# Optimization experiments

Measured on AMD Instinct MI355X. Metric: run time of the kernel, lower is better.

The kernel has to match this reference:

```python
import jax, jax.numpy as jnp
import numpy as np

HEADS = 4
DIM_HEAD = 32
CHUNK = 1024
GROUPS = 8
EPS = 1e-5


def setup_inputs() -> dict:
    key = jax.random.key(0)
    k1, k2, k3 = jax.random.split(key, 3)
    b, dim, h, w = 8, 64, 96, 96
    inner = HEADS * DIM_HEAD  # 128
    x = jax.random.normal(k1, (b, dim, h, w), dtype=jnp.float32)
    W_qkv = jax.random.normal(k2, (3 * inner, dim), dtype=jnp.float32) * (1.0 / np.sqrt(dim))
    W_out = jax.random.normal(k3, (dim, inner), dtype=jnp.float32) * (1.0 / np.sqrt(inner))
    b_out = jnp.zeros((dim,), dtype=jnp.float32)
    gamma = jnp.ones((dim,), dtype=jnp.float32)
    beta = jnp.zeros((dim,), dtype=jnp.float32)
    return {"x": x, "W_qkv": W_qkv, "W_out": W_out, "b_out": b_out,
            "gamma": gamma, "beta": beta}


def reference(x, W_qkv, W_out, b_out, gamma, beta):
    b, c, h, w = x.shape
    n = h * w
    nch = n // CHUNK  # number of full chunks (n chosen divisible by CHUNK)
    d = DIM_HEAD
    BH = b * HEADS

    # 1x1 conv (no bias) == matmul over channel dim
    xf = x.reshape(b, c, n)
    qkv = jnp.einsum('oc,bcn->bon', W_qkv, xf)          # [b, 3*inner, n]
    q, k, v = jnp.split(qkv, 3, axis=1)                  # each [b, inner, n]

    def chunkify(t):
        # [b, inner, n] -> [BH, nch, d, CHUNK]; slicing i:i+CHUNK on last axis
        # equals reshaping n -> (nch, CHUNK) in order.
        return t.reshape(BH, d, nch, CHUNK).transpose(0, 2, 1, 3)

    qc, kc, vc = chunkify(q), chunkify(k), chunkify(v)

    qs = jax.nn.softmax(qc, axis=-1)  # softmax over chunk spatial positions
    ks = jax.nn.softmax(kc, axis=-2)  # softmax over head channels

    # context = k_chunk^T @ v_chunk : [BH, nch, CHUNK, CHUNK]
    ctx = jnp.einsum('gkdi,gkdj->gkij', ks, vc)
    # chunk_out = q_chunk @ context : [BH, nch, d, CHUNK]
    out = jnp.einsum('gkdi,gkij->gkdj', qs, ctx)

    # concat chunks back along spatial dim, reshape to image layout
    out = out.transpose(0, 2, 1, 3).reshape(b, HEADS * d, h, w)

    # to_out: 1x1 conv with bias, then GroupNorm(8, dim)
    y = jnp.einsum('oc,bchw->bohw', W_out, out) + b_out[None, :, None, None]

    yg = y.reshape(b, GROUPS, c // GROUPS, h, w)
    mu = jnp.mean(yg, axis=(2, 3, 4), keepdims=True)
    var = jnp.var(yg, axis=(2, 3, 4), keepdims=True)
    yn = ((yg - mu) * jax.lax.rsqrt(var + EPS)).reshape(b, c, h, w)
    return yn * gamma[None, :, None, None] + beta[None, :, None, None]
```

## Files before the change

### kernel.cpp

```cpp
#include <hip/hip_runtime.h>
#include <hip/hip_bf16.h>

#define N_POS 9216
#define NCHUNK 9
#define BATCH 8
#define CDIM 64
#define HEADS 4
#define EPS 1e-5f

#define PPART_SZ ((size_t)32 * NCHUNK * 1024)
#define NPART 8
#define UBF_BYTES ((size_t)BATCH * NCHUNK * 64 * 128 * 2)
#define WBF_BYTES ((size_t)384 * 64 * 2)

typedef __attribute__((ext_vector_type(8))) short short8;
typedef __attribute__((ext_vector_type(4))) float f32x4;

static __device__ inline unsigned pk2(float a, float b) {
    __hip_bfloat162 h2(__float2bfloat16(a), __float2bfloat16(b));
    return *reinterpret_cast<unsigned*>(&h2);
}
static __device__ inline float bf2f(short s) {
    union { unsigned u; float f; } c; c.u = ((unsigned)(unsigned short)s) << 16; return c.f;
}

__global__ __launch_bounds__(256) void wprep_kernel(const float* __restrict__ Wqkv,
        __hip_bfloat16* __restrict__ wbf, float* __restrict__ stats) {
    int i = blockIdx.x * 256 + threadIdx.x;
    if (i < 6144) {
        float4 v = ((const float4*)Wqkv)[i];
        uint2 u; u.x = pk2(v.x, v.y); u.y = pk2(v.z, v.w);
        ((uint2*)wbf)[i] = u;
    }
    if (i < 128) stats[i] = 0.f;
}

__global__ __launch_bounds__(256) void qkp_kernel(const float* __restrict__ x,
        const __hip_bfloat16* __restrict__ wbf, float* __restrict__ Pparts) {
    int bx = blockIdx.x;
    int b  = blockIdx.y;
    int ck = bx >> 3, pt = bx & 7;
    __shared__ __align__(16) char lraw[36864];
    __hip_bfloat16 (*xs)[72]  = (__hip_bfloat16(*)[72])lraw;
    __hip_bfloat16 (*skT)[72] = (__hip_bfloat16(*)[72])lraw;
    int t = threadIdx.x, w = t >> 6, l = t & 63;
    int l15 = l & 15, quad = l >> 4;

    f32x4 pac[2][2];
    pac[0][0] = (f32x4){0,0,0,0}; pac[0][1] = (f32x4){0,0,0,0};
    pac[1][0] = (f32x4){0,0,0,0}; pac[1][1] = (f32x4){0,0,0,0};

    for (int half = 0; half < 2; ++half) {
        int n0 = bx * 128 + half * 64;
        {
            int p = t & 63, cbase = (t >> 6) * 16;
            const float* xb = x + (size_t)b * CDIM * N_POS + n0 + p;
            #pragma unroll
            for (int j = 0; j < 16; j += 4) {
                float v0 = xb[(size_t)(cbase + j + 0) * N_POS];
                float v1 = xb[(size_t)(cbase + j + 1) * N_POS];
                float v2 = xb[(size_t)(cbase + j + 2) * N_POS];
                float v3 = xb[(size_t)(cbase + j + 3) * N_POS];
                uint2 u; u.x = pk2(v0, v1); u.y = pk2(v2, v3);
                *reinterpret_cast<uint2*>(&xs[p][cbase + j]) = u;
            }
        }
        __syncthreads();

        f32x4 acc[4][4];
        #pragma unroll
        for (int mt = 0; mt < 4; ++mt)
            #pragma unroll
            for (int nt = 0; nt < 4; ++nt) acc[mt][nt] = (f32x4){0.f, 0.f, 0.f, 0.f};
        #pragma unroll
        for (int ks = 0; ks < 2; ++ks) {
            int k0 = ks * 32 + quad * 8;
            short8 av[4];
            #pragma unroll
            for (int mt = 0; mt < 4; ++mt)
                av[mt] = *reinterpret_cast<const short8*>(&xs[mt * 16 + l15][k0]);
            #pragma unroll
            for (int nt = 0; nt < 4; ++nt) {
                short8 bw = *reinterpret_cast<const short8*>(wbf + (size_t)(w * 64 + nt * 16 + l15) * 64 + k0);
                #pragma unroll
                for (int mt = 0; mt < 4; ++mt)
                    acc[mt][nt] = __builtin_amdgcn_mfma_f32_16x16x32_bf16(av[mt], bw, acc[mt][nt], 0, 0, 0);
            }
        }
        __syncthreads();

        #pragma unroll
        for (int nt = 0; nt < 4; ++nt) {
            int ch = w * 64 + nt * 16 + l15;
            #pragma unroll
            for (int mt = 0; mt < 4; ++mt) {
                uint2 u;
                u.x = pk2(acc[mt][nt][0], acc[mt][nt][1]);
                u.y = pk2(acc[mt][nt][2], acc[mt][nt][3]);
                *reinterpret_cast<uint2*>(&skT[ch][mt * 16 + quad * 4]) = u;
            }
        }
        __syncthreads();

        {
            int p = t & 63, h = t >> 6;
            float kr[32]; float mx = -1e30f;
            #pragma unroll
            for (int d = 0; d < 32; ++d) { kr[d] = bf2f(*(const short*)&skT[128 + h * 32 + d][p]); mx = fmaxf(mx, kr[d]); }
            float s = 0.f;
            #pragma unroll
            for (int d = 0; d < 32; ++d) { kr[d] = __expf(kr[d] - mx); s += kr[d]; }
            float is = 1.f / s;
            #pragma unroll
            for (int d = 0; d < 32; ++d) skT[128 + h * 32 + d][p] = __float2bfloat16(kr[d] * is);
            #pragma unroll
            for (int d = 0; d < 32; ++d) {
                float qv = bf2f(*(const short*)&skT[h * 32 + d][p]);
                skT[h * 32 + d][p] = __float2bfloat16(__expf(qv));
            }
        }
        __syncthreads();

        #pragma unroll
        for (int step = 0; step < 2; ++step) {
            int k0 = step * 32 + quad * 8;
            short8 bk[2];
            #pragma unroll
            for (int nt = 0; nt < 2; ++nt)
                bk[nt] = *reinterpret_cast<const short8*>(&skT[128 + w * 32 + nt * 16 + l15][k0]);
            #pragma unroll
            for (int mt = 0; mt < 2; ++mt) {
                short8 aq = *reinterpret_cast<const short8*>(&skT[w * 32 + mt * 16 + l15][k0]);
                pac[mt][0] = __builtin_amdgcn_mfma_f32_16x16x32_bf16(aq, bk[0], pac[mt][0], 0, 0, 0);
                pac[mt][1] = __builtin_amdgcn_mfma_f32_16x16x32_bf16(aq, bk[1], pac[mt][1], 0, 0, 0);
            }
        }
        __syncthreads();
    }

    float* Pp = Pparts + (size_t)pt * PPART_SZ + ((size_t)(b * 4 + w) * NCHUNK + ck) * 1024;
    #pragma unroll
    for (int mt = 0; mt < 2; ++mt)
        #pragma unroll
        for (int nt = 0; nt < 2; ++nt)
            #pragma unroll
            for (int r = 0; r < 4; ++r)
                Pp[(mt * 16 + quad * 4 + r) * 32 + nt * 16 + l15] = pac[mt][nt][r];
}

__global__ __launch_bounds__(256) void umat_kernel(const float* __restrict__ Wout,
        const float* __restrict__ Pparts, __hip_bfloat16* __restrict__ Ubf) {
    int ck = blockIdx.x, b = blockIdx.y, h = blockIdx.z;
    int bh = b * 4 + h;
    int t = threadIdx.x;
    __shared__ float Pl[32][32];
    __shared__ float iZ[32];
    size_t base4 = ((size_t)bh * NCHUNK + ck) * 256;
    {
        const float4* P0 = (const float4*)Pparts + base4 + t;
        float4 s = (float4){0.f, 0.f, 0.f, 0.f};
        #pragma unroll
        for (int j = 0; j < NPART; ++j) {
            float4 a = P0[j * (PPART_SZ / 4)];
            s.x += a.x; s.y += a.y; s.z += a.z; s.w += a.w;
        }
        ((float4*)Pl)[t] = s;
    }
    __syncthreads();
    if (t < 32) {
        float s = 0.f;
        #pragma unroll
        for (int c = 0; c < 32; ++c) s += Pl[t][c];
        iZ[t] = 1.f / s;
    }
    __syncthreads();
    int o = t & 63, wv = t >> 6;
    float wz[32];
    {
        const float4* wr = (const float4*)(Wout + (size_t)o * 128 + h * 32);
        #pragma unroll
        for (int j = 0; j < 8; ++j) {
            float4 f = wr[j];
            wz[j*4+0] = f.x * iZ[j*4+0]; wz[j*4+1] = f.y * iZ[j*4+1];
            wz[j*4+2] = f.z * iZ[j*4+2]; wz[j*4+3] = f.w * iZ[j*4+3];
        }
    }
    float ua[8];
    #pragma unroll
    for (int j = 0; j < 8; ++j) ua[j] = 0.f;
    for (int d = 0; d < 32; ++d) {
        float wd = wz[d];
        #pragma unroll
        for (int j = 0; j < 8; ++j) ua[j] += wd * Pl[d][wv * 8 + j];
    }
    uint4 up;
    up.x = pk2(ua[0], ua[1]); up.y = pk2(ua[2], ua[3]);
    up.z = pk2(ua[4], ua[5]); up.w = pk2(ua[6], ua[7]);
    __hip_bfloat16* Up = Ubf + ((size_t)(b * NCHUNK + ck) * 64 + o) * 128 + h * 32 + wv * 8;
    *reinterpret_cast<uint4*>(Up) = up;
}

__global__ __launch_bounds__(256) void vy_kernel(const float* __restrict__ x,
        const __hip_bfloat16* __restrict__ wbf, const __hip_bfloat16* __restrict__ Ubf,
        const float* __restrict__ bout, __hip_bfloat16* __restrict__ ybf,
        float* __restrict__ stats) {
    int bx = blockIdx.x;
    int b  = blockIdx.y;
    int ck = bx >> 3;
    int n0 = bx * 128;
    __shared__ __align__(16) char lraw[34816];
    __hip_bfloat16 (*xs)[72]    = (__hip_bfloat16(*)[72])lraw;
    __hip_bfloat16 (*vbuf)[136] = (__hip_bfloat16(*)[136])lraw;
    __shared__ float gsum[8], gsq[8];
    int t = threadIdx.x, w = t >> 6, l = t & 63;
    int l15 = l & 15, quad = l >> 4;
    if (t < 8) { gsum[t] = 0.f; gsq[t] = 0.f; }

    {
        int p = t & 127, cbase = (t >> 7) * 32;
        const float* xb = x + (size_t)b * CDIM * N_POS + n0 + p;
        #pragma unroll
        for (int j = 0; j < 32; j += 4) {
            float v0 = xb[(size_t)(cbase + j + 0) * N_POS];
            float v1 = xb[(size_t)(cbase + j + 1) * N_POS];
            float v2 = xb[(size_t)(cbase + j + 2) * N_POS];
            float v3 = xb[(size_t)(cbase + j + 3) * N_POS];
            uint2 u; u.x = pk2(v0, v1); u.y = pk2(v2, v3);
            *reinterpret_cast<uint2*>(&xs[p][cbase + j]) = u;
        }
    }
    __syncthreads();

    int nw = w * 32;
    {
        f32x4 vacc[8][2];
        #pragma unroll
        for (int mt = 0; mt < 8; ++mt) { vacc[mt][0] = (f32x4){0,0,0,0}; vacc[mt][1] = (f32x4){0,0,0,0}; }
        #pragma unroll
        for (int ks = 0; ks < 2; ++ks) {
            int k0 = ks * 32 + quad * 8;
            short8 bfr[2];
            #pragma unroll
            for (int nt = 0; nt < 2; ++nt)
                bfr[nt] = *reinterpret_cast<const short8*>(&xs[nw + nt * 16 + l15][k0]);
            #pragma unroll
            for (int mt = 0; mt < 8; ++mt) {
                short8 afr = *reinterpret_cast<const short8*>(wbf + (size_t)(256 + mt * 16 + l15) * 64 + k0);
                vacc[mt][0] = __builtin_amdgcn_mfma_f32_16x16x32_bf16(afr, bfr[0], vacc[mt][0], 0, 0, 0);
                vacc[mt][1] = __builtin_amdgcn_mfma_f32_16x16x32_bf16(afr, bfr[1], vacc[mt][1], 0, 0, 0);
            }
        }
        __syncthreads();

        #pragma unroll
        for (int mt = 0; mt < 8; ++mt)
            #pragma unroll
            for (int nt = 0; nt < 2; ++nt) {
                int p = nw + nt * 16 + l15;
                uint2 u;
                u.x = pk2(vacc[mt][nt][0], vacc[mt][nt][1]);
                u.y = pk2(vacc[mt][nt][2], vacc[mt][nt][3]);
                *reinterpret_cast<uint2*>(&vbuf[p][mt * 16 + quad * 4]) = u;
            }
    }
    __syncthreads();

    const __hip_bfloat16* Ub = Ubf + (size_t)(b * NCHUNK + ck) * 64 * 128;
    f32x4 acc[4][2];
    #pragma unroll
    for (int mt = 0; mt < 4; ++mt) { acc[mt][0] = (f32x4){0,0,0,0}; acc[mt][1] = (f32x4){0,0,0,0}; }
    #pragma unroll
    for (int ks = 0; ks < 4; ++ks) {
        int k0 = ks * 32 + quad * 8;
        short8 bf[2];
        #pragma unroll
        for (int nt = 0; nt < 2; ++nt)
            bf[nt] = *reinterpret_cast<const short8*>(&vbuf[nw + nt * 16 + l15][k0]);
        #pragma unroll
        for (int mt = 0; mt < 4; ++mt) {
            short8 af = *reinterpret_cast<const short8*>(Ub + (size_t)(mt * 16 + l15) * 128 + k0);
            acc[mt][0] = __builtin_amdgcn_mfma_f32_16x16x32_bf16(af, bf[0], acc[mt][0], 0, 0, 0);
            acc[mt][1] = __builtin_amdgcn_mfma_f32_16x16x32_bf16(af, bf[1], acc[mt][1], 0, 0, 0);
        }
    }
    float gsl[4], gql[4];
    #pragma unroll
    for (int mt = 0; mt < 4; ++mt) { gsl[mt] = 0.f; gql[mt] = 0.f; }
    __hip_bfloat16* yb = ybf + (size_t)b * CDIM * N_POS;
    int nbase = n0 + nw;
    #pragma unroll
    for (int mt = 0; mt < 4; ++mt) {
        float4 bo = *reinterpret_cast<const float4*>(bout + mt * 16 + quad * 4);
        const float* bop = reinterpret_cast<const float*>(&bo);
        #pragma unroll
        for (int nt = 0; nt < 2; ++nt) {
            int n = nbase + nt * 16 + l15;
            #pragma unroll
            for (int r = 0; r < 4; ++r) {
                int o = mt * 16 + quad * 4 + r;
                float val = acc[mt][nt][r] + bop[r];
                yb[(size_t)o * N_POS + n] = __float2bfloat16(val);
                gsl[mt] += val; gql[mt] += val * val;
            }
        }
    }
    #pragma unroll
    for (int off = 16; off >= 1; off >>= 1) {
        #pragma unroll
        for (int mt = 0; mt < 4; ++mt) {
            gsl[mt] += __shfl_xor(gsl[mt], off, 64);
            gql[mt] += __shfl_xor(gql[mt], off, 64);
        }
    }
    if (l == 0 || l == 32) {
        int qh = quad >> 1;
        #pragma unroll
        for (int mt = 0; mt < 4; ++mt) {
            atomicAdd(&gsum[2 * mt + qh], gsl[mt]);
            atomicAdd(&gsq[2 * mt + qh], gql[mt]);
        }
    }
    __syncthreads();
    if (t < 8) {
        atomicAdd(&stats[(b * 8 + t) * 2],     gsum[t]);
        atomicAdd(&stats[(b * 8 + t) * 2 + 1], gsq[t]);
    }
}

__global__ __launch_bounds__(256) void gn_kernel(const __hip_bfloat16* __restrict__ ybf,
        float* __restrict__ out, const float* __restrict__ stats,
        const float* __restrict__ gamma, const float* __restrict__ beta) {
    int bc = blockIdx.y;
    int c = bc & 63, b = bc >> 6;
    int g = c >> 3;
    float s = stats[(b * 8 + g) * 2], q = stats[(b * 8 + g) * 2 + 1];
    const float invN = 1.f / (8.f * N_POS);
    float mean = s * invN;
    float var = q * invN - mean * mean;
    float sc = rsqrtf(var + EPS);
    float ga = gamma[c] * sc;
    float be = beta[c] - mean * sc * gamma[c];
    size_t base = ((size_t)b * CDIM + c) * N_POS + (size_t)(blockIdx.x * 256 + threadIdx.x) * 4;
    uint2 u = *reinterpret_cast<const uint2*>(ybf + base);
    float4 v;
    v.x = bf2f((short)(u.x & 0xffff)); v.y = bf2f((short)(u.x >> 16));
    v.z = bf2f((short)(u.y & 0xffff)); v.w = bf2f((short)(u.y >> 16));
    v.x = v.x * ga + be; v.y = v.y * ga + be; v.z = v.z * ga + be; v.w = v.w * ga + be;
    *reinterpret_cast<float4*>(out + base) = v;
}

extern "C" void kernel_launch(void* const* d_in, const int* in_sizes, int n_in,
                              void* d_out, int out_size, void* d_ws, size_t ws_size,
                              hipStream_t stream) {
    const float* x     = (const float*)d_in[0];
    const float* Wqkv  = (const float*)d_in[1];
    const float* Wout  = (const float*)d_in[2];
    const float* bout  = (const float*)d_in[3];
    const float* gamma = (const float*)d_in[4];
    const float* beta  = (const float*)d_in[5];
    float* out = (float*)d_out;

    float* stats  = (float*)d_ws;
    float* Pparts = stats + 128;
    __hip_bfloat16* Ubf = (__hip_bfloat16*)(Pparts + NPART * PPART_SZ);
    __hip_bfloat16* wbf = (__hip_bfloat16*)((char*)Ubf + UBF_BYTES);
    __hip_bfloat16* ybf = (__hip_bfloat16*)((char*)wbf + WBF_BYTES);

    wprep_kernel<<<dim3(24), 256, 0, stream>>>(Wqkv, wbf, stats);
    qkp_kernel<<<dim3(72, BATCH), 256, 0, stream>>>(x, wbf, Pparts);
    umat_kernel<<<dim3(NCHUNK, BATCH, HEADS), 256, 0, stream>>>(Wout, Pparts, Ubf);
    vy_kernel<<<dim3(72, BATCH), 256, 0, stream>>>(x, wbf, Ubf, bout, ybf, stats);
    gn_kernel<<<dim3(9, 512), 256, 0, stream>>>(ybf, out, stats, gamma, beta);
}
```

Baseline: 125.6 us.

## Reduce chunk partials with atomics and fuse U-matrix build into vy kernel

qkp_kernel now atomically adds its partial 32x32 P tiles into a single zeroed buffer instead of writing eight separate partial slices. The separate umat_kernel is removed, and each vy_kernel block rebuilds the Wout-scaled U matrix for its chunk in shared memory. This drops one launch and the partial-sum and U round trips through global memory. The cost is atomic contention (eight blocks per target), a larger zeroing pass in wprep, redundant U computation in all eight blocks per chunk, and extra LDS in vy_kernel that may reduce occupancy.

```diff
diff --git a/kernel.cpp b/kernel.cpp
--- a/kernel.cpp
+++ b/kernel.cpp
@@ -8,9 +8,7 @@
 #define HEADS 4
 #define EPS 1e-5f
 
-#define PPART_SZ ((size_t)32 * NCHUNK * 1024)
-#define NPART 8
-#define UBF_BYTES ((size_t)BATCH * NCHUNK * 64 * 128 * 2)
+#define PSUM_SZ ((size_t)32 * NCHUNK * 1024)
 #define WBF_BYTES ((size_t)384 * 64 * 2)
 
 typedef __attribute__((ext_vector_type(8))) short short8;
@@ -25,21 +23,22 @@
 }
 
 __global__ __launch_bounds__(256) void wprep_kernel(const float* __restrict__ Wqkv,
-        __hip_bfloat16* __restrict__ wbf, float* __restrict__ stats) {
+        __hip_bfloat16* __restrict__ wbf, float* __restrict__ zbase) {
     int i = blockIdx.x * 256 + threadIdx.x;
     if (i < 6144) {
         float4 v = ((const float4*)Wqkv)[i];
         uint2 u; u.x = pk2(v.x, v.y); u.y = pk2(v.z, v.w);
         ((uint2*)wbf)[i] = u;
     }
-    if (i < 128) stats[i] = 0.f;
+    if (i < (128 + (int)PSUM_SZ) / 4)
+        ((float4*)zbase)[i] = (float4){0.f, 0.f, 0.f, 0.f};
 }
 
 __global__ __launch_bounds__(256) void qkp_kernel(const float* __restrict__ x,
-        const __hip_bfloat16* __restrict__ wbf, float* __restrict__ Pparts) {
+        const __hip_bfloat16* __restrict__ wbf, float* __restrict__ Psum) {
     int bx = blockIdx.x;
     int b  = blockIdx.y;
-    int ck = bx >> 3, pt = bx & 7;
+    int ck = bx >> 3;
     __shared__ __align__(16) char lraw[36864];
     __hip_bfloat16 (*xs)[72]  = (__hip_bfloat16(*)[72])lraw;
     __hip_bfloat16 (*skT)[72] = (__hip_bfloat16(*)[72])lraw;
@@ -138,72 +137,20 @@
         __syncthreads();
     }
 
-    float* Pp = Pparts + (size_t)pt * PPART_SZ + ((size_t)(b * 4 + w) * NCHUNK + ck) * 1024;
+    float* Pp = Psum + ((size_t)(b * 4 + w) * NCHUNK + ck) * 1024;
     #pragma unroll
     for (int mt = 0; mt < 2; ++mt)
         #pragma unroll
         for (int nt = 0; nt < 2; ++nt)
             #pragma unroll
             for (int r = 0; r < 4; ++r)
-                Pp[(mt * 16 + quad * 4 + r) * 32 + nt * 16 + l15] = pac[mt][nt][r];
-}
-
-__global__ __launch_bounds__(256) void umat_kernel(const float* __restrict__ Wout,
-        const float* __restrict__ Pparts, __hip_bfloat16* __restrict__ Ubf) {
-    int ck = blockIdx.x, b = blockIdx.y, h = blockIdx.z;
-    int bh = b * 4 + h;
-    int t = threadIdx.x;
-    __shared__ float Pl[32][32];
-    __shared__ float iZ[32];
-    size_t base4 = ((size_t)bh * NCHUNK + ck) * 256;
-    {
-        const float4* P0 = (const float4*)Pparts + base4 + t;
-        float4 s = (float4){0.f, 0.f, 0.f, 0.f};
-        #pragma unroll
-        for (int j = 0; j < NPART; ++j) {
-            float4 a = P0[j * (PPART_SZ / 4)];
-            s.x += a.x; s.y += a.y; s.z += a.z; s.w += a.w;
-        }
-        ((float4*)Pl)[t] = s;
-    }
-    __syncthreads();
-    if (t < 32) {
-        float s = 0.f;
-        #pragma unroll
-        for (int c = 0; c < 32; ++c) s += Pl[t][c];
-        iZ[t] = 1.f / s;
-    }
-    __syncthreads();
-    int o = t & 63, wv = t >> 6;
-    float wz[32];
-    {
-        const float4* wr = (const float4*)(Wout + (size_t)o * 128 + h * 32);
-        #pragma unroll
-        for (int j = 0; j < 8; ++j) {
-            float4 f = wr[j];
-            wz[j*4+0] = f.x * iZ[j*4+0]; wz[j*4+1] = f.y * iZ[j*4+1];
-            wz[j*4+2] = f.z * iZ[j*4+2]; wz[j*4+3] = f.w * iZ[j*4+3];
-        }
-    }
-    float ua[8];
-    #pragma unroll
-    for (int j = 0; j < 8; ++j) ua[j] = 0.f;
-    for (int d = 0; d < 32; ++d) {
-        float wd = wz[d];
-        #pragma unroll
-        for (int j = 0; j < 8; ++j) ua[j] += wd * Pl[d][wv * 8 + j];
-    }
-    uint4 up;
-    up.x = pk2(ua[0], ua[1]); up.y = pk2(ua[2], ua[3]);
-    up.z = pk2(ua[4], ua[5]); up.w = pk2(ua[6], ua[7]);
-    __hip_bfloat16* Up = Ubf + ((size_t)(b * NCHUNK + ck) * 64 + o) * 128 + h * 32 + wv * 8;
-    *reinterpret_cast<uint4*>(Up) = up;
+                atomicAdd(&Pp[(mt * 16 + quad * 4 + r) * 32 + nt * 16 + l15], pac[mt][nt][r]);
 }
 
 __global__ __launch_bounds__(256) void vy_kernel(const float* __restrict__ x,
-        const __hip_bfloat16* __restrict__ wbf, const __hip_bfloat16* __restrict__ Ubf,
-        const float* __restrict__ bout, __hip_bfloat16* __restrict__ ybf,
-        float* __restrict__ stats) {
+        const __hip_bfloat16* __restrict__ wbf, const float* __restrict__ Psum,
+        const float* __restrict__ Wout, const float* __restrict__ bout,
+        __hip_bfloat16* __restrict__ ybf, float* __restrict__ stats) {
     int bx = blockIdx.x;
     int b  = blockIdx.y;
     int ck = bx >> 3;
@@ -211,10 +158,56 @@
     __shared__ __align__(16) char lraw[34816];
     __hip_bfloat16 (*xs)[72]    = (__hip_bfloat16(*)[72])lraw;
     __hip_bfloat16 (*vbuf)[136] = (__hip_bfloat16(*)[136])lraw;
+    float (*Pl4)[32][32] = (float(*)[32][32])lraw;
+    __shared__ __align__(16) __hip_bfloat16 Ubuf[64][136];
+    __shared__ float iZ4[4][32];
     __shared__ float gsum[8], gsq[8];
     int t = threadIdx.x, w = t >> 6, l = t & 63;
     int l15 = l & 15, quad = l >> 4;
     if (t < 8) { gsum[t] = 0.f; gsq[t] = 0.f; }
+
+    {
+        const float4* Pb = (const float4*)(Psum + ((size_t)b * 4 * NCHUNK + ck) * 1024);
+        #pragma unroll
+        for (int h = 0; h < 4; ++h)
+            ((float4*)Pl4[h])[t] = Pb[(size_t)h * NCHUNK * 256 + t];
+    }
+    __syncthreads();
+    if (t < 128) {
+        int h = t >> 5, d = t & 31;
+        float s = 0.f;
+        #pragma unroll
+        for (int c = 0; c < 32; ++c) s += Pl4[h][d][c];
+        iZ4[h][d] = 1.f / s;
+    }
+    __syncthreads();
+    {
+        int o = t & 63, wv = t >> 6;
+        #pragma unroll
+        for (int h = 0; h < 4; ++h) {
+            float wz[32];
+            const float4* wr = (const float4*)(Wout + (size_t)o * 128 + h * 32);
+            #pragma unroll
+            for (int j = 0; j < 8; ++j) {
+                float4 f = wr[j];
+                wz[j*4+0] = f.x * iZ4[h][j*4+0]; wz[j*4+1] = f.y * iZ4[h][j*4+1];
+                wz[j*4+2] = f.z * iZ4[h][j*4+2]; wz[j*4+3] = f.w * iZ4[h][j*4+3];
+            }
+            float ua[8];
+            #pragma unroll
+            for (int j = 0; j < 8; ++j) ua[j] = 0.f;
+            for (int d = 0; d < 32; ++d) {
+                float wd = wz[d];
+                #pragma unroll
+                for (int j = 0; j < 8; ++j) ua[j] += wd * Pl4[h][d][wv * 8 + j];
+            }
+            uint4 up;
+            up.x = pk2(ua[0], ua[1]); up.y = pk2(ua[2], ua[3]);
+            up.z = pk2(ua[4], ua[5]); up.w = pk2(ua[6], ua[7]);
+            *reinterpret_cast<uint4*>(&Ubuf[o][h * 32 + wv * 8]) = up;
+        }
+    }
+    __syncthreads();
 
     {
         int p = t & 127, cbase = (t >> 7) * 32;
@@ -265,7 +258,6 @@
     }
     __syncthreads();
 
-    const __hip_bfloat16* Ub = Ubf + (size_t)(b * NCHUNK + ck) * 64 * 128;
     f32x4 acc[4][2];
     #pragma unroll
     for (int mt = 0; mt < 4; ++mt) { acc[mt][0] = (f32x4){0,0,0,0}; acc[mt][1] = (f32x4){0,0,0,0}; }
@@ -278,7 +270,7 @@
             bf[nt] = *reinterpret_cast<const short8*>(&vbuf[nw + nt * 16 + l15][k0]);
         #pragma unroll
         for (int mt = 0; mt < 4; ++mt) {
-            short8 af = *reinterpret_cast<const short8*>(Ub + (size_t)(mt * 16 + l15) * 128 + k0);
+            short8 af = *reinterpret_cast<const short8*>(&Ubuf[mt * 16 + l15][k0]);
             acc[mt][0] = __builtin_amdgcn_mfma_f32_16x16x32_bf16(af, bf[0], acc[mt][0], 0, 0, 0);
             acc[mt][1] = __builtin_amdgcn_mfma_f32_16x16x32_bf16(af, bf[1], acc[mt][1], 0, 0, 0);
         }
@@ -360,15 +352,13 @@
     const float* beta  = (const float*)d_in[5];
     float* out = (float*)d_out;
 
-    float* stats  = (float*)d_ws;
-    float* Pparts = stats + 128;
-    __hip_bfloat16* Ubf = (__hip_bfloat16*)(Pparts + NPART * PPART_SZ);
-    __hip_bfloat16* wbf = (__hip_bfloat16*)((char*)Ubf + UBF_BYTES);
+    float* stats = (float*)d_ws;
+    float* Psum  = stats + 128;
+    __hip_bfloat16* wbf = (__hip_bfloat16*)(Psum + PSUM_SZ);
     __hip_bfloat16* ybf = (__hip_bfloat16*)((char*)wbf + WBF_BYTES);
 
-    wprep_kernel<<<dim3(24), 256, 0, stream>>>(Wqkv, wbf, stats);
-    qkp_kernel<<<dim3(72, BATCH), 256, 0, stream>>>(x, wbf, Pparts);
-    umat_kernel<<<dim3(NCHUNK, BATCH, HEADS), 256, 0, stream>>>(Wout, Pparts, Ubf);
-    vy_kernel<<<dim3(72, BATCH), 256, 0, stream>>>(x, wbf, Ubf, bout, ybf, stats);
+    wprep_kernel<<<dim3(289), 256, 0, stream>>>(Wqkv, wbf, stats);
+    qkp_kernel<<<dim3(72, BATCH), 256, 0, stream>>>(x, wbf, Psum);
+    vy_kernel<<<dim3(72, BATCH), 256, 0, stream>>>(x, wbf, Psum, Wout, bout, ybf, stats);
     gn_kernel<<<dim3(9, 512), 256, 0, stream>>>(ybf, out, stats, gamma, beta);
 }
```

Measured after the change: 138.0 us. 1.1x slower.
